# Optimization experiments

Measured on AMD Instinct MI355X. Metric: run time of the kernel, lower is better.

## Reference

```python
import jax, jax.numpy as jnp
import numpy as np

ALPHA = 0.2        # LeakyReLU slope
NEG_BIG = -9e15    # mask fill value from the original module


def setup_inputs() -> dict:
    key = jax.random.key(0)
    k1, k2, k3, k4 = jax.random.split(key, 4)
    N, F_IN, F_OUT = 8192, 256, 128
    h = jax.random.normal(k1, (N, F_IN), dtype=jnp.float32)
    adj = jax.random.randint(k2, (N, N), 0, 2, dtype=jnp.int32)
    W = jax.random.normal(k3, (F_IN, F_OUT), dtype=jnp.float32) * (1.0 / np.sqrt(F_IN))
    a = jax.random.normal(k4, (2 * F_OUT, 1), dtype=jnp.float32) * (1.0 / np.sqrt(2 * F_OUT))
    return {"h": h, "adj": adj, "W": W, "a": a}


def reference(h, adj, W, a):
    f_out = W.shape[1]
    Wh = h @ W                                   # [N, F_out]
    Wh1 = Wh @ a[:f_out, :]                      # [N, 1]
    Wh2 = Wh @ a[f_out:, :]                      # [N, 1]
    e = Wh1 + Wh2.T                              # [N, N] broadcast-add
    e = jnp.where(e > 0, e, ALPHA * e)           # LeakyReLU
    e = jnp.where(adj > 0, e, NEG_BIG)           # adjacency mask
    attention = jax.nn.softmax(e, axis=-1)       # row softmax
    # dropout rate = 0.0 -> identity
    h_prime = attention @ Wh                     # [N, F_out]
    return jax.nn.elu(h_prime)
```

## Files before the change

### kernel.cpp

```cpp
#include <hip/hip_runtime.h>

#define NV 8192
#define FIN 256
#define FOUT 128

typedef __bf16 bf16_t;
typedef __attribute__((ext_vector_type(8))) __bf16 bf16x8;
typedef __attribute__((ext_vector_type(16))) float f32x16;

__global__ __launch_bounds__(256) void wh_kernel(
    const float* __restrict__ h, const float* __restrict__ W,
    const float* __restrict__ a,
    bf16_t* __restrict__ WhbT, float* __restrict__ Wh1, float* __restrict__ Wh2)
{
  __shared__ float As[64][34];
  __shared__ float Bs[64][128];
  __shared__ float Cs[32][129];
  __shared__ float red1[32][16];
  __shared__ float red2[32][16];
  const int t  = threadIdx.x;
  const int i0 = blockIdx.x * 32;
  const int c  = t & 15;
  const int r  = t >> 4;
  float acc0[8], acc1[8];
  #pragma unroll
  for (int j = 0; j < 8; j++) { acc0[j] = 0.f; acc1[j] = 0.f; }

  for (int k0 = 0; k0 < FIN; k0 += 64) {
    {
      const int ia = t >> 3;
      const int ka = (t & 7) * 8;
      const float* src = h + (size_t)(i0 + ia) * FIN + k0 + ka;
      float4 v0 = *(const float4*)src;
      float4 v1 = *(const float4*)(src + 4);
      As[ka+0][ia]=v0.x; As[ka+1][ia]=v0.y; As[ka+2][ia]=v0.z; As[ka+3][ia]=v0.w;
      As[ka+4][ia]=v1.x; As[ka+5][ia]=v1.y; As[ka+6][ia]=v1.z; As[ka+7][ia]=v1.w;
    }
    {
      const int kb = t >> 2;
      const int cb = (t & 3) * 32;
      const float4* src = (const float4*)(W + (size_t)(k0 + kb) * FOUT + cb);
      float4* dst = (float4*)&Bs[kb][cb];
      #pragma unroll
      for (int q = 0; q < 8; q++) dst[q] = src[q];
    }
    __syncthreads();
    #pragma unroll 4
    for (int k = 0; k < 64; k++) {
      float2 av = *(const float2*)&As[k][r*2];
      float b[8];
      *(float4*)&b[0] = *(const float4*)&Bs[k][c*8];
      *(float4*)&b[4] = *(const float4*)&Bs[k][c*8+4];
      #pragma unroll
      for (int j = 0; j < 8; j++) {
        acc0[j] = fmaf(av.x, b[j], acc0[j]);
        acc1[j] = fmaf(av.y, b[j], acc1[j]);
      }
    }
    __syncthreads();
  }

  float p1a = 0.f, p2a = 0.f, p1b = 0.f, p2b = 0.f;
  #pragma unroll
  for (int j = 0; j < 8; j++) {
    Cs[r*2][c*8+j]   = acc0[j];
    Cs[r*2+1][c*8+j] = acc1[j];
    float w1 = a[c*8+j];
    float w2 = a[FOUT + c*8+j];
    p1a = fmaf(acc0[j], w1, p1a); p2a = fmaf(acc0[j], w2, p2a);
    p1b = fmaf(acc1[j], w1, p1b); p2b = fmaf(acc1[j], w2, p2b);
  }
  red1[r*2][c]   = p1a; red2[r*2][c]   = p2a;
  red1[r*2+1][c] = p1b; red2[r*2+1][c] = p2b;
  __syncthreads();
  if (t < 32) {
    float s = 0.f;
    #pragma unroll
    for (int q = 0; q < 16; q++) s += red1[t][q];
    Wh1[i0 + t] = s;
  } else if (t < 64) {
    float s = 0.f;
    #pragma unroll
    for (int q = 0; q < 16; q++) s += red2[t-32][q];
    Wh2[i0 + t - 32] = s;
  }
  {
    const int f = t & 127, half = t >> 7;
    union { bf16_t b[16]; uint4 v[2]; } pk;
    #pragma unroll
    for (int q = 0; q < 16; q++) pk.b[q] = (bf16_t)Cs[half*16 + q][f];
    uint4* dst = (uint4*)(WhbT + (size_t)f * NV + i0 + half*16);
    dst[0] = pk.v[0]; dst[1] = pk.v[1];
  }
}

__global__ __launch_bounds__(256) void attn_kernel(
    const int* __restrict__ adj, const bf16_t* __restrict__ WhbT,
    const float* __restrict__ Wh1v, const float* __restrict__ Wh2v,
    float* __restrict__ nump, float* __restrict__ denp)
{
  __shared__ bf16_t Plds[64][72];
  __shared__ bf16_t Blds[128][72];
  __shared__ float denlds[64][4];
  const int t     = threadIdx.x;
  const int rb    = blockIdx.x >> 2;
  const int split = blockIdx.x & 3;
  const int i0 = rb * 64;
  const int j0 = split * 2048;
  const int il = t >> 2;
  const int jg = (t & 3) * 16;
  const float wh1 = Wh1v[i0 + il];
  const int lane = t & 63;
  const int w    = t >> 6;
  const int rh = (w & 1) * 32;
  const int ch = (w >> 1) * 64;
  const int ml = lane & 31;
  const int kh = (lane >> 5) * 8;
  f32x16 acc0 = {};
  f32x16 acc1 = {};
  float den_t = 0.f;

  for (int jc = 0; jc < 2048; jc += 64) {
    const int jb = j0 + jc;
    __syncthreads();
    {
      const int n  = t >> 1;
      const int hf = (t & 1) * 32;
      const uint4* s4 = (const uint4*)(WhbT + (size_t)n * NV + jb + hf);
      uint4* dst = (uint4*)&Blds[n][hf];
      dst[0] = s4[0]; dst[1] = s4[1]; dst[2] = s4[2]; dst[3] = s4[3];
    }
    {
      const int* arow = adj + (size_t)(i0 + il) * NV + jb + jg;
      int4 a0 = *(const int4*)arow;
      int4 a1 = *(const int4*)(arow + 4);
      int4 a2 = *(const int4*)(arow + 8);
      int4 a3 = *(const int4*)(arow + 12);
      float4 w0 = *(const float4*)(Wh2v + jb + jg);
      float4 w1 = *(const float4*)(Wh2v + jb + jg + 4);
      float4 w2 = *(const float4*)(Wh2v + jb + jg + 8);
      float4 w3 = *(const float4*)(Wh2v + jb + jg + 12);
      const int am[16] = {a0.x,a0.y,a0.z,a0.w, a1.x,a1.y,a1.z,a1.w,
                          a2.x,a2.y,a2.z,a2.w, a3.x,a3.y,a3.z,a3.w};
      const float wm[16] = {w0.x,w0.y,w0.z,w0.w, w1.x,w1.y,w1.z,w1.w,
                            w2.x,w2.y,w2.z,w2.w, w3.x,w3.y,w3.z,w3.w};
      bf16x8 pv0, pv1;
      #pragma unroll
      for (int q = 0; q < 16; q++) {
        float e = wh1 + wm[q];
        e = fmaxf(e, 0.2f * e);
        float p = (am[q] > 0) ? __expf(e) : 0.0f;
        den_t += p;
        if (q < 8) pv0[q] = (bf16_t)p; else pv1[q-8] = (bf16_t)p;
      }
      *(bf16x8*)&Plds[il][jg]     = pv0;
      *(bf16x8*)&Plds[il][jg + 8] = pv1;
    }
    __syncthreads();
    #pragma unroll
    for (int ks = 0; ks < 4; ks++) {
      const int k = ks * 16 + kh;
      bf16x8 af = *(const bf16x8*)&Plds[rh + ml][k];
      bf16x8 b0 = *(const bf16x8*)&Blds[ch + ml][k];
      bf16x8 b1 = *(const bf16x8*)&Blds[ch + 32 + ml][k];
      acc0 = __builtin_amdgcn_mfma_f32_32x32x16_bf16(af, b0, acc0, 0, 0, 0);
      acc1 = __builtin_amdgcn_mfma_f32_32x32x16_bf16(af, b1, acc1, 0, 0, 0);
    }
  }

  denlds[il][t & 3] = den_t;
  __syncthreads();
  if (t < 64) {
    denp[(size_t)split * NV + i0 + t] =
        denlds[t][0] + denlds[t][1] + denlds[t][2] + denlds[t][3];
  }
  float* base = nump + ((size_t)split * NV + i0) * FOUT;
  const int col = ch + ml;
  const int r4  = 4 * (lane >> 5);
  #pragma unroll
  for (int reg = 0; reg < 16; reg++) {
    const int row = rh + (reg & 3) + 8 * (reg >> 2) + r4;
    base[(size_t)row * FOUT + col]      = acc0[reg];
    base[(size_t)row * FOUT + col + 32] = acc1[reg];
  }
}

__global__ __launch_bounds__(256) void finalize_kernel(
    const float* __restrict__ nump, const float* __restrict__ denp,
    float* __restrict__ out)
{
  const int gid = blockIdx.x * 256 + threadIdx.x;
  const int i  = gid >> 5;
  const int f0 = (gid & 31) * 4;
  const float den = denp[i] + denp[NV + i] + denp[2*NV + i] + denp[3*NV + i];
  float4 s = make_float4(0.f, 0.f, 0.f, 0.f);
  #pragma unroll
  for (int sp = 0; sp < 4; sp++) {
    float4 v = *(const float4*)&nump[((size_t)sp * NV + i) * FOUT + f0];
    s.x += v.x; s.y += v.y; s.z += v.z; s.w += v.w;
  }
  const float inv = 1.0f / den;
  float4 r;
  r.x = s.x * inv; r.y = s.y * inv; r.z = s.z * inv; r.w = s.w * inv;
  r.x = r.x > 0.f ? r.x : __expf(r.x) - 1.0f;
  r.y = r.y > 0.f ? r.y : __expf(r.y) - 1.0f;
  r.z = r.z > 0.f ? r.z : __expf(r.z) - 1.0f;
  r.w = r.w > 0.f ? r.w : __expf(r.w) - 1.0f;
  *(float4*)&out[(size_t)i * FOUT + f0] = r;
}

extern "C" void kernel_launch(void* const* d_in, const int* in_sizes, int n_in,
                              void* d_out, int out_size, void* d_ws, size_t ws_size,
                              hipStream_t stream) {
  const float* h  = (const float*)d_in[0];
  const int*  adj = (const int*)d_in[1];
  const float* W  = (const float*)d_in[2];
  const float* a  = (const float*)d_in[3];
  float* out = (float*)d_out;
  char* ws = (char*)d_ws;
  bf16_t* WhbT = (bf16_t*)ws;
  float* Wh1  = (float*)(ws + 2097152);
  float* Wh2  = (float*)(ws + 2097152 + 32768);
  float* denp = (float*)(ws + 2097152 + 65536);
  float* nump = (float*)(ws + 2097152 + 65536 + 131072);

  wh_kernel<<<256, 256, 0, stream>>>(h, W, a, WhbT, Wh1, Wh2);
  attn_kernel<<<512, 256, 0, stream>>>(adj, WhbT, Wh1, Wh2, nump, denp);
  finalize_kernel<<<1024, 256, 0, stream>>>(nump, denp, out);
}
```

Baseline: 420.1 us.

## Rewrite attention kernel to load adj straight into MFMA registers with prefetch

The attention kernel drops LDS staging. Each lane now loads its own adjacency row and builds the bf16 probability A-fragment directly in registers, while B fragments are read from global WhbT without going through shared memory. Adjacency loads are double-buffered in registers so the next 64-column chunk is in flight while the current one is processed. Blocks now cover 128 rows with 4 N-blocks per wave and 8 column splits, which means larger nump partials and more finalize reads. This trades extra register pressure (launch bounds set to 2) and uncoalesced global B loads for removing barriers and LDS traffic.

```diff
diff --git a/kernel.cpp b/kernel.cpp
--- a/kernel.cpp
+++ b/kernel.cpp
@@ -3,6 +3,8 @@
 #define NV 8192
 #define FIN 256
 #define FOUT 128
+#define SPLITS 8
+#define PANEL 1024
 
 typedef __bf16 bf16_t;
 typedef __attribute__((ext_vector_type(8))) __bf16 bf16x8;
@@ -94,94 +96,88 @@
   }
 }
 
-__global__ __launch_bounds__(256) void attn_kernel(
+#define LOAD8(buf, off) do {                                                  \
+    _Pragma("unroll")                                                         \
+    for (int ks = 0; ks < 4; ks++) {                                          \
+      buf[ks*2]   = *(const int4*)(rowp + (off) + ks*16 + hi8);               \
+      buf[ks*2+1] = *(const int4*)(rowp + (off) + ks*16 + hi8 + 4);           \
+    } } while (0)
+
+#define PROCESS(buf, jc) do {                                                 \
+    const int jbL = j0 + (jc);                                                \
+    bf16x8 af[4];                                                             \
+    _Pragma("unroll")                                                         \
+    for (int ks = 0; ks < 4; ks++) {                                          \
+      float4 wA = *(const float4*)(Wh2v + jbL + ks*16 + hi8);                 \
+      float4 wB = *(const float4*)(Wh2v + jbL + ks*16 + hi8 + 4);             \
+      const float wm[8] = {wA.x,wA.y,wA.z,wA.w, wB.x,wB.y,wB.z,wB.w};         \
+      const int4 aa = buf[ks*2], ab = buf[ks*2+1];                            \
+      const int am[8] = {aa.x,aa.y,aa.z,aa.w, ab.x,ab.y,ab.z,ab.w};           \
+      _Pragma("unroll")                                                       \
+      for (int q = 0; q < 8; q++) {                                           \
+        float e = wh1 + wm[q];                                                \
+        e = fmaxf(e, 0.2f * e);                           \
+        float p = (am[q] > 0) ? __expf(e) : 0.0f;             \
+        den_t += p;                                                           \
+        af[ks][q] = (bf16_t)p;                                                \
+      }                                                                       \
+    }                                                                         \
+    _Pragma("unroll")                                                         \
+    for (int nb = 0; nb < 4; nb++) {                                          \
+      _Pragma("unroll")                                                       \
+      for (int ks = 0; ks < 4; ks++) {                                        \
+        bf16x8 bfv = *(const bf16x8*)(bp + (size_t)(nb*32 + ml) * NV          \
+                                      + (jc) + ks*16 + hi8);                  \
+        acc[nb] = __builtin_amdgcn_mfma_f32_32x32x16_bf16(af[ks], bfv,        \
+                                                          acc[nb], 0, 0, 0); \
+      }                                                                       \
+    } } while (0)
+
+__global__ __launch_bounds__(256, 2) void attn_kernel(
     const int* __restrict__ adj, const bf16_t* __restrict__ WhbT,
     const float* __restrict__ Wh1v, const float* __restrict__ Wh2v,
     float* __restrict__ nump, float* __restrict__ denp)
 {
-  __shared__ bf16_t Plds[64][72];
-  __shared__ bf16_t Blds[128][72];
-  __shared__ float denlds[64][4];
   const int t     = threadIdx.x;
-  const int rb    = blockIdx.x >> 2;
-  const int split = blockIdx.x & 3;
-  const int i0 = rb * 64;
-  const int j0 = split * 2048;
-  const int il = t >> 2;
-  const int jg = (t & 3) * 16;
-  const float wh1 = Wh1v[i0 + il];
-  const int lane = t & 63;
-  const int w    = t >> 6;
-  const int rh = (w & 1) * 32;
-  const int ch = (w >> 1) * 64;
-  const int ml = lane & 31;
-  const int kh = (lane >> 5) * 8;
-  f32x16 acc0 = {};
-  f32x16 acc1 = {};
+  const int lane  = t & 63;
+  const int w     = t >> 6;
+  const int ml    = lane & 31;
+  const int hi    = lane >> 5;
+  const int hi8   = hi * 8;
+  const int rb    = blockIdx.x >> 3;
+  const int split = blockIdx.x & 7;
+  const int i0    = rb * 128;
+  const int j0    = split * PANEL;
+  const int row   = i0 + w * 32 + ml;
+  const float wh1 = Wh1v[row];
+  const int* rowp = adj + (size_t)row * NV + j0;
+  const bf16_t* bp = WhbT + j0;
+  f32x16 acc[4] = {};
   float den_t = 0.f;
-
-  for (int jc = 0; jc < 2048; jc += 64) {
-    const int jb = j0 + jc;
-    __syncthreads();
-    {
-      const int n  = t >> 1;
-      const int hf = (t & 1) * 32;
-      const uint4* s4 = (const uint4*)(WhbT + (size_t)n * NV + jb + hf);
-      uint4* dst = (uint4*)&Blds[n][hf];
-      dst[0] = s4[0]; dst[1] = s4[1]; dst[2] = s4[2]; dst[3] = s4[3];
-    }
-    {
-      const int* arow = adj + (size_t)(i0 + il) * NV + jb + jg;
-      int4 a0 = *(const int4*)arow;
-      int4 a1 = *(const int4*)(arow + 4);
-      int4 a2 = *(const int4*)(arow + 8);
-      int4 a3 = *(const int4*)(arow + 12);
-      float4 w0 = *(const float4*)(Wh2v + jb + jg);
-      float4 w1 = *(const float4*)(Wh2v + jb + jg + 4);
-      float4 w2 = *(const float4*)(Wh2v + jb + jg + 8);
-      float4 w3 = *(const float4*)(Wh2v + jb + jg + 12);
-      const int am[16] = {a0.x,a0.y,a0.z,a0.w, a1.x,a1.y,a1.z,a1.w,
-                          a2.x,a2.y,a2.z,a2.w, a3.x,a3.y,a3.z,a3.w};
-      const float wm[16] = {w0.x,w0.y,w0.z,w0.w, w1.x,w1.y,w1.z,w1.w,
-                            w2.x,w2.y,w2.z,w2.w, w3.x,w3.y,w3.z,w3.w};
-      bf16x8 pv0, pv1;
-      #pragma unroll
-      for (int q = 0; q < 16; q++) {
-        float e = wh1 + wm[q];
-        e = fmaxf(e, 0.2f * e);
-        float p = (am[q] > 0) ? __expf(e) : 0.0f;
-        den_t += p;
-        if (q < 8) pv0[q] = (bf16_t)p; else pv1[q-8] = (bf16_t)p;
-      }
-      *(bf16x8*)&Plds[il][jg]     = pv0;
-      *(bf16x8*)&Plds[il][jg + 8] = pv1;
-    }
-    __syncthreads();
-    #pragma unroll
-    for (int ks = 0; ks < 4; ks++) {
-      const int k = ks * 16 + kh;
-      bf16x8 af = *(const bf16x8*)&Plds[rh + ml][k];
-      bf16x8 b0 = *(const bf16x8*)&Blds[ch + ml][k];
-      bf16x8 b1 = *(const bf16x8*)&Blds[ch + 32 + ml][k];
-      acc0 = __builtin_amdgcn_mfma_f32_32x32x16_bf16(af, b0, acc0, 0, 0, 0);
-      acc1 = __builtin_amdgcn_mfma_f32_32x32x16_bf16(af, b1, acc1, 0, 0, 0);
-    }
-  }
-
-  denlds[il][t & 3] = den_t;
-  __syncthreads();
-  if (t < 64) {
-    denp[(size_t)split * NV + i0 + t] =
-        denlds[t][0] + denlds[t][1] + denlds[t][2] + denlds[t][3];
-  }
-  float* base = nump + ((size_t)split * NV + i0) * FOUT;
-  const int col = ch + ml;
-  const int r4  = 4 * (lane >> 5);
-  #pragma unroll
-  for (int reg = 0; reg < 16; reg++) {
-    const int row = rh + (reg & 3) + 8 * (reg >> 2) + r4;
-    base[(size_t)row * FOUT + col]      = acc0[reg];
-    base[(size_t)row * FOUT + col + 32] = acc1[reg];
+  int4 c0[8], c1[8];
+
+  LOAD8(c0, 0);
+  #pragma unroll 1
+  for (int jc = 0; jc < PANEL; jc += 128) {
+    LOAD8(c1, jc + 64);
+    PROCESS(c0, jc);
+    const int off2 = (jc + 128 < PANEL) ? jc + 128 : 0;
+    LOAD8(c0, off2);
+    PROCESS(c1, jc + 64);
+  }
+
+  den_t += __shfl(den_t, lane ^ 32, 64);
+  if (hi == 0) denp[(size_t)split * NV + row] = den_t;
+
+  float* base = nump + ((size_t)split * NV + i0 + w * 32) * FOUT;
+  const int r4 = 4 * hi;
+  #pragma unroll
+  for (int nb = 0; nb < 4; nb++) {
+    #pragma unroll
+    for (int reg = 0; reg < 16; reg++) {
+      const int crow = (reg & 3) + 8 * (reg >> 2) + r4;
+      base[(size_t)crow * FOUT + nb * 32 + ml] = acc[nb][reg];
+    }
   }
 }
 
@@ -192,16 +188,18 @@
   const int gid = blockIdx.x * 256 + threadIdx.x;
   const int i  = gid >> 5;
   const int f0 = (gid & 31) * 4;
-  const float den = denp[i] + denp[NV + i] + denp[2*NV + i] + denp[3*NV + i];
-  float4 s = make_float4(0.f, 0.f, 0.f, 0.f);
-  #pragma unroll
-  for (int sp = 0; sp < 4; sp++) {
-    float4 v = *(const float4*)&nump[((size_t)sp * NV + i) * FOUT + f0];
-    s.x += v.x; s.y += v.y; s.z += v.z; s.w += v.w;
+  float den = 0.f;
+  #pragma unroll
+  for (int s = 0; s < SPLITS; s++) den += denp[(size_t)s * NV + i];
+  float4 sv = make_float4(0.f, 0.f, 0.f, 0.f);
+  #pragma unroll
+  for (int s = 0; s < SPLITS; s++) {
+    float4 v = *(const float4*)&nump[((size_t)s * NV + i) * FOUT + f0];
+    sv.x += v.x; sv.y += v.y; sv.z += v.z; sv.w += v.w;
   }
   const float inv = 1.0f / den;
   float4 r;
-  r.x = s.x * inv; r.y = s.y * inv; r.z = s.z * inv; r.w = s.w * inv;
+  r.x = sv.x * inv; r.y = sv.y * inv; r.z = sv.z * inv; r.w = sv.w * inv;
   r.x = r.x > 0.f ? r.x : __expf(r.x) - 1.0f;
   r.y = r.y > 0.f ? r.y : __expf(r.y) - 1.0f;
   r.z = r.z > 0.f ? r.z : __expf(r.z) - 1.0f;
@@ -222,7 +220,7 @@
   float* Wh1  = (float*)(ws + 2097152);
   float* Wh2  = (float*)(ws + 2097152 + 32768);
   float* denp = (float*)(ws + 2097152 + 65536);
-  float* nump = (float*)(ws + 2097152 + 65536 + 131072);
+  float* nump = (float*)(ws + 2097152 + 65536 + 262144);
 
   wh_kernel<<<256, 256, 0, stream>>>(h, W, a, WhbT, Wh1, Wh2);
   attn_kernel<<<512, 256, 0, stream>>>(adj, WhbT, Wh1, Wh2, nump, denp);
```

Result: slower. 477.3 us (+13.6%).
